# Optimization experiments

Measured on AMD Instinct MI355X. Metric: run time of the kernel, lower is better.

The kernel has to match this reference:

```python
import jax, jax.numpy as jnp
import numpy as np

N = 65536    # collocation points
N1 = 1024    # RBF centers
EPS = 0.1    # multiscale parameter used for width init scale


def setup_inputs() -> dict:
    key = jax.random.key(0)
    ks = jax.random.split(key, 10)
    x = jax.random.uniform(ks[0], (N, 2), dtype=jnp.float32)

    def mk(i):
        h = jax.random.uniform(ks[3 * i + 1], (N1,), dtype=jnp.float32)
        c = jax.random.uniform(ks[3 * i + 2], (N1, 2), dtype=jnp.float32)
        w = 5.0 * jax.random.uniform(ks[3 * i + 3], (N1, 2), dtype=jnp.float32) / EPS
        return h, c, w

    h1, c1, w1 = mk(0)
    h2, c2, w2 = mk(1)
    h3, c3, w3 = mk(2)
    return dict(x=x, hight=h1, center=c1, width=w1,
                hight2=h2, center2=c2, width2=w2,
                hight3=h3, center3=c3, width3=w3)


def _rbf(X, c, h, w):
    """Gaussian RBF expansion. X:(N,2) points, c:(N1,2) centers,
    h:(N1,) heights, w:(N1,2) widths. Returns u, du/dx, du/dy, each (N,)."""
    x1 = X[:, 0:1] - c[None, :, 0]          # (N, N1)
    y1 = X[:, 1:2] - c[None, :, 1]          # (N, N1)
    d1 = w[:, 0] ** 2                        # (N1,)
    d2 = w[:, 1] ** 2                        # (N1,)
    e = jnp.exp(-(x1 ** 2) * d1 - (y1 ** 2) * d2)  # (N, N1)
    u = e @ h                                # (N,)
    ux = (-2.0 * x1 * d1 * e) @ h            # (N,)
    uy = (-2.0 * y1 * d2 * e) @ h            # (N,)
    return u, ux, uy


def reference(x, hight, center, width, hight2, center2, width2,
              hight3, center3, width3):
    _, ux, uy = _rbf(x, center, hight, width)
    P, Px, _ = _rbf(x, center2, hight2, width2)
    Q, _, Qy = _rbf(x, center3, hight3, width3)
    return (ux, uy, P, Px, Q, Qy)
```

## Files before the change

### kernel.cpp

```cpp
#include <hip/hip_runtime.h>
#include <math.h>

#define N_PTS 65536
#define N_CTR 1024

#if __has_builtin(__builtin_amdgcn_exp2f)
#define EXP2(x) __builtin_amdgcn_exp2f(x)
#else
#define EXP2(x) exp2f(x)
#endif

__global__ __launch_bounds__(256) void srbf_kernel(
    const float* __restrict__ x,
    const float* __restrict__ h0, const float* __restrict__ c0, const float* __restrict__ w0,
    const float* __restrict__ h1, const float* __restrict__ c1, const float* __restrict__ w1,
    const float* __restrict__ h2, const float* __restrict__ c2, const float* __restrict__ w2,
    float* __restrict__ out)
{
    __shared__ float4 s4[N_CTR];
    __shared__ float2 s2[N_CTR];

    const int set = blockIdx.x >> 8;
    const int blk = blockIdx.x & 255;
    const int tid = threadIdx.x;

    const float* __restrict__ h = (set == 0) ? h0 : ((set == 1) ? h1 : h2);
    const float2* __restrict__ c = (const float2*)((set == 0) ? c0 : ((set == 1) ? c1 : c2));
    const float2* __restrict__ w = (const float2*)((set == 0) ? w0 : ((set == 1) ? w1 : w2));

    const float LOG2E = 1.4426950408889634f;

    for (int j = tid; j < N_CTR; j += 256) {
        float2 cj = c[j];
        float2 wj = w[j];
        float hh = h[j];
        float d1 = wj.x * wj.x;
        float d2 = wj.y * wj.y;
        s4[j] = make_float4(cj.x, cj.y, -d1 * LOG2E, -d2 * LOG2E);
        float a, b;
        if (set == 0)      { a = -2.f * hh * d1; b = -2.f * hh * d2; }
        else if (set == 1) { a = hh;             b = -2.f * hh * d1; }
        else               { a = hh;             b = -2.f * hh * d2; }
        s2[j] = make_float2(a, b);
    }
    __syncthreads();

    const int i = (blk << 8) + tid;
    const float2 xy = ((const float2*)x)[i];
    const float xi = xy.x, yi = xy.y;

    float acc0 = 0.f, acc1 = 0.f;

    if (set == 0) {
        #pragma unroll 8
        for (int j = 0; j < N_CTR; ++j) {
            float4 v = s4[j];
            float2 g = s2[j];
            float dx = xi - v.x, dy = yi - v.y;
            float s = fmaf(dy * dy, v.w, dx * dx * v.z);
            float e = EXP2(s);
            acc0 = fmaf(dx * g.x, e, acc0);
            acc1 = fmaf(dy * g.y, e, acc1);
        }
    } else if (set == 1) {
        #pragma unroll 8
        for (int j = 0; j < N_CTR; ++j) {
            float4 v = s4[j];
            float2 g = s2[j];
            float dx = xi - v.x, dy = yi - v.y;
            float s = fmaf(dy * dy, v.w, dx * dx * v.z);
            float e = EXP2(s);
            acc0 = fmaf(g.x, e, acc0);
            acc1 = fmaf(dx * g.y, e, acc1);
        }
    } else {
        #pragma unroll 8
        for (int j = 0; j < N_CTR; ++j) {
            float4 v = s4[j];
            float2 g = s2[j];
            float dx = xi - v.x, dy = yi - v.y;
            float s = fmaf(dy * dy, v.w, dx * dx * v.z);
            float e = EXP2(s);
            acc0 = fmaf(g.x, e, acc0);
            acc1 = fmaf(dy * g.y, e, acc1);
        }
    }

    float* o = out + (size_t)set * 2 * N_PTS;
    o[i] = acc0;
    o[N_PTS + i] = acc1;
}

extern "C" void kernel_launch(void* const* d_in, const int* in_sizes, int n_in,
                              void* d_out, int out_size, void* d_ws, size_t ws_size,
                              hipStream_t stream) {
    const float* x  = (const float*)d_in[0];
    const float* h1 = (const float*)d_in[1];
    const float* c1 = (const float*)d_in[2];
    const float* w1 = (const float*)d_in[3];
    const float* h2 = (const float*)d_in[4];
    const float* c2 = (const float*)d_in[5];
    const float* w2 = (const float*)d_in[6];
    const float* h3 = (const float*)d_in[7];
    const float* c3 = (const float*)d_in[8];
    const float* w3 = (const float*)d_in[9];

    srbf_kernel<<<dim3(3 * 256), dim3(256), 0, stream>>>(
        x, h1, c1, w1, h2, c2, w2, h3, c3, w3, (float*)d_out);
}
```

Measured before the change: 59.46 us.

## Expand Gaussian exponent into polynomial form and split centers across blocks with atomics

Rewrites the exponent as a polynomial in x and y with per-center precomputed coefficients, so the inner loop needs only four FMAs before exp2 and no per-center subtraction. The derivative terms are split so that the multiply by x or y happens once after the loop. Each thread now handles two points, and the center dimension is split into four chunks across blocks. Partial sums are combined with atomicAdd into an output cleared by a memset. The expanded form can lose precision through cancellation when widths are large, and the change adds a memset launch and atomic traffic.

Result: slower. 62.51 us (+5.1%).

```diff
diff --git a/kernel.cpp b/kernel.cpp
--- a/kernel.cpp
+++ b/kernel.cpp
@@ -3,6 +3,8 @@
 
 #define N_PTS 65536
 #define N_CTR 1024
+#define CHUNK 256
+#define PPB   512
 
 #if __has_builtin(__builtin_amdgcn_exp2f)
 #define EXP2(x) __builtin_amdgcn_exp2f(x)
@@ -17,78 +19,124 @@
     const float* __restrict__ h2, const float* __restrict__ c2, const float* __restrict__ w2,
     float* __restrict__ out)
 {
-    __shared__ float4 s4[N_CTR];
-    __shared__ float2 s2[N_CTR];
+    __shared__ float4 sA[CHUNK];
+    __shared__ float4 sB[CHUNK];
+    __shared__ float  sC[CHUNK];
 
-    const int set = blockIdx.x >> 8;
-    const int blk = blockIdx.x & 255;
-    const int tid = threadIdx.x;
+    const int bid   = blockIdx.x;
+    const int set   = bid >> 9;
+    const int r     = bid & 511;
+    const int chunk = r >> 7;
+    const int pblk  = r & 127;
+    const int tid   = threadIdx.x;
 
-    const float* __restrict__ h = (set == 0) ? h0 : ((set == 1) ? h1 : h2);
+    const float*  __restrict__ h = (set == 0) ? h0 : ((set == 1) ? h1 : h2);
     const float2* __restrict__ c = (const float2*)((set == 0) ? c0 : ((set == 1) ? c1 : c2));
     const float2* __restrict__ w = (const float2*)((set == 0) ? w0 : ((set == 1) ? w1 : w2));
 
     const float LOG2E = 1.4426950408889634f;
 
-    for (int j = tid; j < N_CTR; j += 256) {
+    {
+        const int j = chunk * CHUNK + tid;
         float2 cj = c[j];
         float2 wj = w[j];
-        float hh = h[j];
+        float  hh = h[j];
         float d1 = wj.x * wj.x;
         float d2 = wj.y * wj.y;
-        s4[j] = make_float4(cj.x, cj.y, -d1 * LOG2E, -d2 * LOG2E);
-        float a, b;
-        if (set == 0)      { a = -2.f * hh * d1; b = -2.f * hh * d2; }
-        else if (set == 1) { a = hh;             b = -2.f * hh * d1; }
-        else               { a = hh;             b = -2.f * hh * d2; }
-        s2[j] = make_float2(a, b);
+        float zb =  2.f * cj.x * d1 * LOG2E;
+        float zc = -d1 * LOG2E;
+        float zd =  2.f * cj.y * d2 * LOG2E;
+        float ze = -d2 * LOG2E;
+        float za = -(cj.x * cj.x * d1 + cj.y * cj.y * d2) * LOG2E;
+        float k0, k1, k2, k3;
+        if (set == 0) {
+            k0 = -2.f * hh * d1;
+            k1 =  2.f * hh * d1 * cj.x;
+            k2 = -2.f * hh * d2;
+            k3 =  2.f * hh * d2 * cj.y;
+        } else if (set == 1) {
+            k0 = hh;
+            k1 = -2.f * hh * d1;
+            k2 =  2.f * hh * d1 * cj.x;
+            k3 = 0.f;
+        } else {
+            k0 = hh;
+            k1 = -2.f * hh * d2;
+            k2 =  2.f * hh * d2 * cj.y;
+            k3 = 0.f;
+        }
+        sA[tid] = make_float4(zb, zc, zd, ze);
+        sB[tid] = make_float4(za, k0, k1, k2);
+        sC[tid] = k3;
     }
     __syncthreads();
 
-    const int i = (blk << 8) + tid;
-    const float2 xy = ((const float2*)x)[i];
-    const float xi = xy.x, yi = xy.y;
-
-    float acc0 = 0.f, acc1 = 0.f;
+    const int i0 = pblk * PPB + tid;
+    const int i1 = i0 + 256;
+    const float2 Pa = ((const float2*)x)[i0];
+    const float2 Pb = ((const float2*)x)[i1];
+    const float xa = Pa.x, ya = Pa.y, xb = Pb.x, yb = Pb.y;
+    const float xa2 = xa * xa, ya2 = ya * ya, xb2 = xb * xb, yb2 = yb * yb;
 
     if (set == 0) {
-        #pragma unroll 8
-        for (int j = 0; j < N_CTR; ++j) {
-            float4 v = s4[j];
-            float2 g = s2[j];
-            float dx = xi - v.x, dy = yi - v.y;
-            float s = fmaf(dy * dy, v.w, dx * dx * v.z);
-            float e = EXP2(s);
-            acc0 = fmaf(dx * g.x, e, acc0);
-            acc1 = fmaf(dy * g.y, e, acc1);
+        float aP0 = 0.f, aQ0 = 0.f, aP1 = 0.f, aQ1 = 0.f;
+        float bP0 = 0.f, bQ0 = 0.f, bP1 = 0.f, bQ1 = 0.f;
+        #pragma unroll 4
+        for (int jj = 0; jj < CHUNK; ++jj) {
+            float4 A = sA[jj];
+            float4 B = sB[jj];
+            float  k3 = sC[jj];
+            float sa = fmaf(xa, A.x, B.x);
+            sa = fmaf(xa2, A.y, sa);
+            sa = fmaf(ya,  A.z, sa);
+            sa = fmaf(ya2, A.w, sa);
+            float sb = fmaf(xb, A.x, B.x);
+            sb = fmaf(xb2, A.y, sb);
+            sb = fmaf(yb,  A.z, sb);
+            sb = fmaf(yb2, A.w, sb);
+            float ea = EXP2(sa);
+            float eb = EXP2(sb);
+            aP0 = fmaf(B.y, ea, aP0);  aQ0 = fmaf(B.z, ea, aQ0);
+            aP1 = fmaf(B.w, ea, aP1);  aQ1 = fmaf(k3,  ea, aQ1);
+            bP0 = fmaf(B.y, eb, bP0);  bQ0 = fmaf(B.z, eb, bQ0);
+            bP1 = fmaf(B.w, eb, bP1);  bQ1 = fmaf(k3,  eb, bQ1);
         }
-    } else if (set == 1) {
-        #pragma unroll 8
-        for (int j = 0; j < N_CTR; ++j) {
-            float4 v = s4[j];
-            float2 g = s2[j];
-            float dx = xi - v.x, dy = yi - v.y;
-            float s = fmaf(dy * dy, v.w, dx * dx * v.z);
-            float e = EXP2(s);
-            acc0 = fmaf(g.x, e, acc0);
-            acc1 = fmaf(dx * g.y, e, acc1);
+        atomicAdd(&out[i0],          fmaf(xa, aP0, aQ0));
+        atomicAdd(&out[N_PTS + i0],  fmaf(ya, aP1, aQ1));
+        atomicAdd(&out[i1],          fmaf(xb, bP0, bQ0));
+        atomicAdd(&out[N_PTS + i1],  fmaf(yb, bP1, bQ1));
+    } else {
+        float aU = 0.f, aP = 0.f, aQ = 0.f;
+        float bU = 0.f, bP = 0.f, bQ = 0.f;
+        #pragma unroll 4
+        for (int jj = 0; jj < CHUNK; ++jj) {
+            float4 A = sA[jj];
+            float4 B = sB[jj];
+            float sa = fmaf(xa, A.x, B.x);
+            sa = fmaf(xa2, A.y, sa);
+            sa = fmaf(ya,  A.z, sa);
+            sa = fmaf(ya2, A.w, sa);
+            float sb = fmaf(xb, A.x, B.x);
+            sb = fmaf(xb2, A.y, sb);
+            sb = fmaf(yb,  A.z, sb);
+            sb = fmaf(yb2, A.w, sb);
+            float ea = EXP2(sa);
+            float eb = EXP2(sb);
+            aU = fmaf(B.y, ea, aU);
+            aP = fmaf(B.z, ea, aP);
+            aQ = fmaf(B.w, ea, aQ);
+            bU = fmaf(B.y, eb, bU);
+            bP = fmaf(B.z, eb, bP);
+            bQ = fmaf(B.w, eb, bQ);
         }
-    } else {
-        #pragma unroll 8
-        for (int j = 0; j < N_CTR; ++j) {
-            float4 v = s4[j];
-            float2 g = s2[j];
-            float dx = xi - v.x, dy = yi - v.y;
-            float s = fmaf(dy * dy, v.w, dx * dx * v.z);
-            float e = EXP2(s);
-            acc0 = fmaf(g.x, e, acc0);
-            acc1 = fmaf(dy * g.y, e, acc1);
-        }
+        float* o = out + (size_t)set * 2 * N_PTS;
+        const float ga = (set == 1) ? xa : ya;
+        const float gb = (set == 1) ? xb : yb;
+        atomicAdd(&o[i0],         aU);
+        atomicAdd(&o[N_PTS + i0], fmaf(ga, aP, aQ));
+        atomicAdd(&o[i1],         bU);
+        atomicAdd(&o[N_PTS + i1], fmaf(gb, bP, bQ));
     }
-
-    float* o = out + (size_t)set * 2 * N_PTS;
-    o[i] = acc0;
-    o[N_PTS + i] = acc1;
 }
 
 extern "C" void kernel_launch(void* const* d_in, const int* in_sizes, int n_in,
@@ -105,6 +153,8 @@
     const float* c3 = (const float*)d_in[8];
     const float* w3 = (const float*)d_in[9];
 
-    srbf_kernel<<<dim3(3 * 256), dim3(256), 0, stream>>>(
+    hipMemsetAsync(d_out, 0, (size_t)out_size * sizeof(float), stream);
+
+    srbf_kernel<<<dim3(3 * 4 * 128), dim3(256), 0, stream>>>(
         x, h1, c1, w1, h2, c2, w2, h3, c3, w3, (float*)d_out);
 }
```
